# Kernel optimization log

Hardware: AMD Instinct MI355X
Metric: run time of the kernel (lower is better)

## Reference

```python
import jax, jax.numpy as jnp
import numpy as np

EPS = 1e-6

def setup_inputs() -> dict:
    key = jax.random.key(0)
    k1, k2, k3 = jax.random.split(key, 3)
    D = 1024
    return {
        "x": jax.random.normal(k1, (2, 2048, D), dtype=jnp.float32),
        "w_norm": jnp.ones((D,), dtype=jnp.float32),
        "w_qkv": jax.random.normal(k2, (3 * D, D), dtype=jnp.float32) * (1.0 / np.sqrt(D)),
        "w_out": jax.random.normal(k3, (D, D), dtype=jnp.float32) * (1.0 / np.sqrt(D)),
        "window_size": 128,
        "n_heads": 16,
    }

def reference(x, w_norm, w_qkv, w_out, window_size, n_heads):
    B, L, D = x.shape
    H = n_heads
    dh = D // H
    skip = x
    # RMSNorm
    rms = jnp.sqrt(jnp.mean(x * x, axis=-1, keepdims=True) + EPS)
    xn = w_norm * (x / rms)
    # QKV projection (torch Linear: y = x @ W.T)
    qkv = xn @ w_qkv.T  # [B, L, 3D]
    q, k, v = jnp.split(qkv, 3, axis=-1)
    q = q.reshape(B, L, H, dh).transpose(0, 2, 1, 3)  # [B,H,L,dh]
    k = k.reshape(B, L, H, dh).transpose(0, 2, 1, 3)
    v = v.reshape(B, L, H, dh).transpose(0, 2, 1, 3)
    scores = jnp.einsum("bhid,bhjd->bhij", q, k) / np.sqrt(dh)  # [B,H,L,L]
    # Symmetric window: token i attends to j in [i - w//2, i + w//2]
    idx = jnp.arange(L)
    half = window_size // 2
    band = jnp.abs(idx[:, None] - idx[None, :]) <= half  # [L, L]
    scores = jnp.where(band, scores, -jnp.inf)
    attn = jax.nn.softmax(scores, axis=-1)  # zeros outside band, matches torch loop
    out = jnp.einsum("bhij,bhjd->bhid", attn, v)  # [B,H,L,dh]
    out = out.transpose(0, 2, 1, 3).reshape(B, L, D)
    out = out @ w_out.T
    return out + skip
```

## Files before the change

kernel.cpp:

```cpp
#include <hip/hip_runtime.h>
#include <hip/hip_bf16.h>
#include <cstdint>

typedef float f32x4 __attribute__((ext_vector_type(4)));
typedef float f32x16 __attribute__((ext_vector_type(16)));
typedef short s16x8 __attribute__((ext_vector_type(8)));
typedef short s16x4 __attribute__((ext_vector_type(4)));
typedef unsigned int u32x2 __attribute__((ext_vector_type(2)));
typedef unsigned int u32x4 __attribute__((ext_vector_type(4)));

constexpr int B_ = 2, L_ = 2048, D_ = 1024, H_ = 16, DH = 64, HALF = 64;
constexpr int M_ROWS = B_ * L_;
constexpr int QKV_N = 3 * D_;

__device__ __forceinline__ void gload16(const void* g, void* l) {
    __builtin_amdgcn_global_load_lds(
        (const __attribute__((address_space(1))) unsigned int*)g,
        (__attribute__((address_space(3))) unsigned int*)l, 16, 0, 0);
}

__device__ __forceinline__ void cfence() {
    __builtin_amdgcn_sched_barrier(0);
    asm volatile("" ::: "memory");
}

__global__ __launch_bounds__(256) void prep_kernel(const float* __restrict__ x,
                                                   const float* __restrict__ wn,
                                                   const float* __restrict__ wq,
                                                   const float* __restrict__ wo,
                                                   __hip_bfloat16* __restrict__ xn,
                                                   __hip_bfloat16* __restrict__ oq,
                                                   __hip_bfloat16* __restrict__ oo) {
    constexpr int NQ4 = QKV_N * D_ / 4;
    constexpr int NCVT = NQ4 + D_ * D_ / 4;
    constexpr int CVTBLK = NCVT / 256;
    int bid = blockIdx.x;
    if (bid < CVTBLK) {
        int i = bid * 256 + threadIdx.x;
        const float* src; __hip_bfloat16* dst; int j;
        if (i < NQ4) { src = wq; dst = oq; j = i; }
        else         { src = wo; dst = oo; j = i - NQ4; }
        float4 v = reinterpret_cast<const float4*>(src)[j];
        s16x4 pk;
        float vals[4] = {v.x, v.y, v.z, v.w};
#pragma unroll
        for (int e = 0; e < 4; ++e) {
            __hip_bfloat16 t = __float2bfloat16(vals[e]);
            pk[e] = *reinterpret_cast<short*>(&t);
        }
        *(s16x4*)(dst + (size_t)j * 4) = pk;
    } else {
        int w = threadIdx.x >> 6, lane = threadIdx.x & 63;
        int row = (bid - CVTBLK) * 4 + w;
        const float4* xr = reinterpret_cast<const float4*>(x + (size_t)row * D_);
        const float4* wr = reinterpret_cast<const float4*>(wn);
        float4 v[4];
        float ss = 0.f;
#pragma unroll
        for (int c = 0; c < 4; ++c) {
            v[c] = xr[c * 64 + lane];
            ss += v[c].x * v[c].x + v[c].y * v[c].y + v[c].z * v[c].z + v[c].w * v[c].w;
        }
#pragma unroll
        for (int off = 32; off; off >>= 1) ss += __shfl_xor(ss, off);
        float rinv = rsqrtf(ss * (1.0f / D_) + 1e-6f);
#pragma unroll
        for (int c = 0; c < 4; ++c) {
            float4 wv = wr[c * 64 + lane];
            s16x4 pk;
            float vals[4] = {v[c].x * rinv * wv.x, v[c].y * rinv * wv.y,
                             v[c].z * rinv * wv.z, v[c].w * rinv * wv.w};
#pragma unroll
            for (int e = 0; e < 4; ++e) {
                __hip_bfloat16 t = __float2bfloat16(vals[e]);
                pk[e] = *reinterpret_cast<short*>(&t);
            }
            *(s16x4*)(xn + (size_t)row * D_ + (c * 64 + lane) * 4) = pk;
        }
    }
}

template <int EPI, int BN, int MINW>
__global__ __launch_bounds__(256, MINW) void gemm_pipe_kernel(const __hip_bfloat16* __restrict__ A,
                                                              const __hip_bfloat16* __restrict__ Bt,
                                                              __hip_bfloat16* __restrict__ Cbf,
                                                              __hip_bfloat16* __restrict__ vT,
                                                              float* __restrict__ Cf,
                                                              const float* __restrict__ resid,
                                                              int M, int N, int K) {
    constexpr int BM = 128;
    constexpr int NFR = BN / 32;
    constexpr int ATILE = BM * 64;
    constexpr int BTILE = BN * 64;
    constexpr int BUFB = ATILE + BTILE;
    constexpr int AISS = BM / 64, BISS = BN / 64;
    __shared__ __align__(16) char smem[4 * BUFB];

    const int tid = threadIdx.x;
    const int lane = tid & 63;
    const int wid = tid >> 6;

    int nwg = gridDim.x * gridDim.y;
    int lin = blockIdx.y * gridDim.x + blockIdx.x;
    int cpx = nwg >> 3;
    int swz = (lin & 7) * cpx + (lin >> 3);
    int bx = swz % gridDim.x;
    int by = swz / gridDim.x;

    const int rowBase = by * BM;
    const int colBase = bx * BN;
    const int NTILES = K >> 5;

    const int u = (tid & 7) ^ ((tid >> 3) & 7);
    const int sRow = 2 * (tid >> 3) + (u >> 2);
    const int sCol = (u & 3) * 8;
    const __hip_bfloat16* aG = A + (size_t)(rowBase + sRow) * K + sCol;
    const __hip_bfloat16* bG = Bt + (size_t)(colBase + sRow) * K + sCol;
    const int dstW = wid << 10;

    const int wm = wid >> 1, wn = wid & 1;
    const int l15 = lane & 15, hi = lane >> 4;
    const int sRd = (((l15 & 1) << 2) | hi) ^ ((l15 >> 1) & 7);
    const int aRd = wm * 4096 + (l15 >> 1) * 128 + sRd * 16;
    const int bRd = ATILE + wn * (BN * 32) + (l15 >> 1) * 128 + sRd * 16;

    f32x4 acc[4][NFR];
#pragma unroll
    for (int m = 0; m < 4; ++m)
#pragma unroll
        for (int n = 0; n < NFR; ++n) acc[m][n] = (f32x4){0.f, 0.f, 0.f, 0.f};

    auto STAGE = [&](int tt) {
        char* base = smem + ((tt & 3) * BUFB) + dstW;
        const __hip_bfloat16* as = aG + (size_t)tt * 32;
        const __hip_bfloat16* bs = bG + (size_t)tt * 32;
#pragma unroll
        for (int j = 0; j < AISS; ++j)
            gload16(as + (size_t)(j * 64) * K, base + j * 4096);
#pragma unroll
        for (int j = 0; j < BISS; ++j)
            gload16(bs + (size_t)(j * 64) * K, base + ATILE + j * 4096);
    };

    STAGE(0);
    STAGE(1);

    for (int t = 0; t < NTILES; ++t) {
        if (t + 2 < NTILES) {
            STAGE(t + 2);
            if constexpr (AISS + BISS == 4)
                asm volatile("s_waitcnt vmcnt(8)" ::: "memory");
            else
                asm volatile("s_waitcnt vmcnt(6)" ::: "memory");
        } else if (t + 1 < NTILES) {
            if constexpr (AISS + BISS == 4)
                asm volatile("s_waitcnt vmcnt(4)" ::: "memory");
            else
                asm volatile("s_waitcnt vmcnt(3)" ::: "memory");
        } else {
            asm volatile("s_waitcnt vmcnt(0)" ::: "memory");
        }
        asm volatile("s_waitcnt lgkmcnt(0)" ::: "memory");
        __builtin_amdgcn_s_barrier();
        cfence();

        const char* tb = smem + ((t & 3) * BUFB);
        s16x8 af[4], bf[NFR];
#pragma unroll
        for (int mf = 0; mf < 4; ++mf)
            af[mf] = *(const s16x8*)(tb + aRd + mf * 1024);
#pragma unroll
        for (int nf = 0; nf < NFR; ++nf)
            bf[nf] = *(const s16x8*)(tb + bRd + nf * 1024);

        __builtin_amdgcn_s_setprio(1);
#pragma unroll
        for (int mf = 0; mf < 4; ++mf)
#pragma unroll
            for (int nf = 0; nf < NFR; ++nf)
                acc[mf][nf] = __builtin_amdgcn_mfma_f32_16x16x32_bf16(af[mf], bf[nf],
                                                                      acc[mf][nf], 0, 0, 0);
        __builtin_amdgcn_s_setprio(0);
    }

    if constexpr (EPI == 0) {
        if (colBase < 2 * D_) {
#pragma unroll
            for (int mf = 0; mf < 4; ++mf)
#pragma unroll
                for (int nf = 0; nf < NFR; ++nf) {
                    int col = colBase + wn * (BN / 2) + nf * 16 + l15;
                    int row0 = rowBase + wm * 64 + mf * 16 + 4 * hi;
#pragma unroll
                    for (int r = 0; r < 4; ++r)
                        Cbf[(size_t)(row0 + r) * N + col] = __float2bfloat16(acc[mf][nf][r]);
                }
        } else {
            char* Ct = smem;
#pragma unroll
            for (int mf = 0; mf < 4; ++mf)
#pragma unroll
                for (int nf = 0; nf < NFR; ++nf) {
                    int cl = wn * (BN / 2) + nf * 16 + l15;
#pragma unroll
                    for (int r = 0; r < 4; ++r) {
                        int rl = wm * 64 + mf * 16 + 4 * hi + r;
                        __hip_bfloat16 t = __float2bfloat16(acc[mf][nf][r]);
                        *(short*)(Ct + cl * 272 + rl * 2) = *reinterpret_cast<short*>(&t);
                    }
                }
            __syncthreads();
            int cl = tid >> 1, half = tid & 1;
            int gcol = colBase + cl - 2 * D_;
            int hh = gcol >> 6, dd = gcol & 63;
            int bb2 = rowBase >> 11, i0 = rowBase & (L_ - 1);
            __hip_bfloat16* dstp = vT + ((size_t)(bb2 * H_ + hh) * DH + dd) * L_ + i0 + half * 64;
#pragma unroll
            for (int ch = 0; ch < 8; ++ch) {
                s16x8 vv = *(const s16x8*)(Ct + cl * 272 + half * 128 + ch * 16);
                *(s16x8*)(dstp + ch * 8) = vv;
            }
        }
    } else {
#pragma unroll
        for (int mf = 0; mf < 4; ++mf)
#pragma unroll
            for (int nf = 0; nf < NFR; ++nf) {
                int col = colBase + wn * (BN / 2) + nf * 16 + l15;
                int row0 = rowBase + wm * 64 + mf * 16 + 4 * hi;
#pragma unroll
                for (int r = 0; r < 4; ++r)
                    Cf[(size_t)(row0 + r) * N + col] = acc[mf][nf][r] + resid[(size_t)(row0 + r) * N + col];
            }
    }
}

__global__ __launch_bounds__(128, 2) void attn_mfma_kernel(const __hip_bfloat16* __restrict__ qkv,
                                                           const __hip_bfloat16* __restrict__ vT,
                                                           __hip_bfloat16* __restrict__ attn) {
    int tid = threadIdx.x;
    int w = tid >> 6;
    int lane = tid & 63;
    int l31 = lane & 31, hi1 = lane >> 5;
    int tq = blockIdx.x, h = blockIdx.y, b = blockIdx.z;
    int qbase = tq * 64 + 32 * w;
    int kb = qbase - HALF;
    int qg = qbase + l31;
    const __hip_bfloat16* qkvb = qkv + (size_t)(b * L_) * QKV_N;
    const __hip_bfloat16* vTg = vT + (size_t)(b * H_ + h) * DH * L_;

    s16x8 qf[4];
#pragma unroll
    for (int kk = 0; kk < 4; ++kk)
        qf[kk] = *(const s16x8*)(qkvb + (size_t)qg * QKV_N + h * DH + kk * 16 + hi1 * 8);

    f32x16 T[5];
#pragma unroll
    for (int kt = 0; kt < 5; ++kt) T[kt] = (f32x16)(0.f);
#pragma unroll
    for (int kt = 0; kt < 5; ++kt) {
        int keyg = kb + 32 * kt + l31;
        int kc = keyg < 0 ? 0 : (keyg > L_ - 1 ? L_ - 1 : keyg);
        const __hip_bfloat16* kp = qkvb + (size_t)kc * QKV_N + D_ + h * DH + hi1 * 8;
#pragma unroll
        for (int kk = 0; kk < 4; ++kk) {
            s16x8 kf = *(const s16x8*)(kp + kk * 16);
            T[kt] = __builtin_amdgcn_mfma_f32_32x32x16_bf16(kf, qf[kk], T[kt], 0, 0, 0);
        }
    }

    float mx = -1e30f;
#pragma unroll
    for (int kt = 0; kt < 5; ++kt) {
#pragma unroll
        for (int r = 0; r < 16; ++r) {
            int koff = (r & 3) + 8 * (r >> 2) + 4 * hi1;
            int keyg = kb + 32 * kt + koff;
            int del = keyg - qg;
            bool ok = (del >= -HALF) && (del <= HALF) && (keyg >= 0) && (keyg < L_);
            float t = ok ? T[kt][r] * 0.125f : -1e30f;
            T[kt][r] = t;
            mx = fmaxf(mx, t);
        }
    }
    mx = fmaxf(mx, __shfl_xor(mx, 32));
    float sum = 0.f;
#pragma unroll
    for (int kt = 0; kt < 5; ++kt) {
#pragma unroll
        for (int r = 0; r < 16; ++r) {
            float p = __expf(T[kt][r] - mx);
            T[kt][r] = p;
            sum += p;
        }
    }
    sum += __shfl_xor(sum, 32);
    float inv = 1.0f / sum;

    u32x4 pu[10];
#pragma unroll
    for (int kt = 0; kt < 5; ++kt) {
#pragma unroll
        for (int s = 0; s < 2; ++s) {
            unsigned P0, P1, P2, P3;
            asm("v_cvt_pk_bf16_f32 %0, %1, %2" : "=v"(P0) : "v"(T[kt][8 * s + 0]), "v"(T[kt][8 * s + 1]));
            asm("v_cvt_pk_bf16_f32 %0, %1, %2" : "=v"(P1) : "v"(T[kt][8 * s + 2]), "v"(T[kt][8 * s + 3]));
            asm("v_cvt_pk_bf16_f32 %0, %1, %2" : "=v"(P2) : "v"(T[kt][8 * s + 4]), "v"(T[kt][8 * s + 5]));
            asm("v_cvt_pk_bf16_f32 %0, %1, %2" : "=v"(P3) : "v"(T[kt][8 * s + 6]), "v"(T[kt][8 * s + 7]));
            u32x2 sA = __builtin_amdgcn_permlane32_swap(P0, P2, false, false);
            u32x2 sB = __builtin_amdgcn_permlane32_swap(P1, P3, false, false);
            pu[2 * kt + s] = (u32x4){sA[0], sB[0], sA[1], sB[1]};
        }
    }

    f32x16 O[2];
#pragma unroll
    for (int dt = 0; dt < 2; ++dt) O[dt] = (f32x16)(0.f);
#pragma unroll
    for (int t = 0; t < 10; ++t) {
        int kv = kb + 16 * t + 8 * hi1;
        kv = kv < 0 ? 0 : (kv > L_ - 8 ? L_ - 8 : kv);
        s16x8 pf = __builtin_bit_cast(s16x8, pu[t]);
#pragma unroll
        for (int dt = 0; dt < 2; ++dt) {
            s16x8 vf = *(const s16x8*)(vTg + (size_t)(32 * dt + l31) * L_ + kv);
            O[dt] = __builtin_amdgcn_mfma_f32_32x32x16_bf16(vf, pf, O[dt], 0, 0, 0);
        }
    }

    __hip_bfloat16* ob = attn + (size_t)(b * L_ + qg) * D_ + h * DH;
#pragma unroll
    for (int dt = 0; dt < 2; ++dt) {
#pragma unroll
        for (int rr = 0; rr < 4; ++rr) {
            s16x4 pk4;
#pragma unroll
            for (int j = 0; j < 4; ++j) {
                __hip_bfloat16 tb = __float2bfloat16(O[dt][4 * rr + j] * inv);
                pk4[j] = *reinterpret_cast<short*>(&tb);
            }
            *(s16x4*)(ob + 32 * dt + 8 * rr + 4 * hi1) = pk4;
        }
    }
}

extern "C" void kernel_launch(void* const* d_in, const int* in_sizes, int n_in,
                              void* d_out, int out_size, void* d_ws, size_t ws_size,
                              hipStream_t stream) {
    const float* x      = (const float*)d_in[0];
    const float* w_norm = (const float*)d_in[1];
    const float* w_qkv  = (const float*)d_in[2];
    const float* w_out  = (const float*)d_in[3];

    char* ws = (char*)d_ws;
    __hip_bfloat16* xn   = (__hip_bfloat16*)(ws);
    __hip_bfloat16* wq   = (__hip_bfloat16*)(ws + (8u  << 20));
    __hip_bfloat16* wo   = (__hip_bfloat16*)(ws + (14u << 20));
    __hip_bfloat16* qkv  = (__hip_bfloat16*)(ws + (16u << 20));
    __hip_bfloat16* attn = (__hip_bfloat16*)(ws + (40u << 20));
    __hip_bfloat16* vT   = (__hip_bfloat16*)(ws + (48u << 20));
    float* out = (float*)d_out;

    prep_kernel<<<4096 + M_ROWS / 4, 256, 0, stream>>>(x, w_norm, w_qkv, w_out, xn, wq, wo);

    gemm_pipe_kernel<0, 128, 2><<<dim3(QKV_N / 128, M_ROWS / 128), 256, 0, stream>>>(
        xn, wq, qkv, vT, nullptr, nullptr, M_ROWS, QKV_N, D_);

    attn_mfma_kernel<<<dim3(L_ / 64, H_, B_), 128, 0, stream>>>(qkv, vT, attn);

    gemm_pipe_kernel<1, 64, 3><<<dim3(D_ / 64, M_ROWS / 128), 256, 0, stream>>>(
        attn, wo, nullptr, nullptr, out, x, M_ROWS, D_, D_);
}
```

Before: 88.90 us.

## Enlarge QKV GEMM to 256x256 tiles with 512 threads and new LDS swizzle

Splits the templated GEMM into a dedicated QKV kernel and a projection kernel. The QKV kernel moves from 128x128 tiles with 256 threads to 256x256 tiles with 512 threads and 8x4 MFMA fragments per wave, which raises arithmetic intensity and cuts global and LDS traffic per flop. Its V-transpose epilogue now runs in two LDS passes. Both kernels switch to a new XOR swizzle for staging and fragment reads, aimed at LDS bank conflicts. The QKV grid shrinks to 12x16=192 blocks, and the 128 KB LDS footprint may limit occupancy, which risks leaving CUs underused on a large GPU.

```diff
diff --git a/kernel.cpp b/kernel.cpp
--- a/kernel.cpp
+++ b/kernel.cpp
@@ -80,20 +80,13 @@
     }
 }
 
-template <int EPI, int BN, int MINW>
-__global__ __launch_bounds__(256, MINW) void gemm_pipe_kernel(const __hip_bfloat16* __restrict__ A,
-                                                              const __hip_bfloat16* __restrict__ Bt,
-                                                              __hip_bfloat16* __restrict__ Cbf,
-                                                              __hip_bfloat16* __restrict__ vT,
-                                                              float* __restrict__ Cf,
-                                                              const float* __restrict__ resid,
-                                                              int M, int N, int K) {
-    constexpr int BM = 128;
-    constexpr int NFR = BN / 32;
-    constexpr int ATILE = BM * 64;
-    constexpr int BTILE = BN * 64;
-    constexpr int BUFB = ATILE + BTILE;
-    constexpr int AISS = BM / 64, BISS = BN / 64;
+__global__ __launch_bounds__(512, 2) void gemm_qkv_kernel(const __hip_bfloat16* __restrict__ A,
+                                                          const __hip_bfloat16* __restrict__ Bt,
+                                                          __hip_bfloat16* __restrict__ Cbf,
+                                                          __hip_bfloat16* __restrict__ vT,
+                                                          int M, int N, int K) {
+    constexpr int ATILE = 16384;
+    constexpr int BUFB = 32768;
     __shared__ __align__(16) char smem[4 * BUFB];
 
     const int tid = threadIdx.x;
@@ -107,56 +100,47 @@
     int bx = swz % gridDim.x;
     int by = swz / gridDim.x;
 
-    const int rowBase = by * BM;
-    const int colBase = bx * BN;
-    const int NTILES = K >> 5;
-
-    const int u = (tid & 7) ^ ((tid >> 3) & 7);
-    const int sRow = 2 * (tid >> 3) + (u >> 2);
-    const int sCol = (u & 3) * 8;
-    const __hip_bfloat16* aG = A + (size_t)(rowBase + sRow) * K + sCol;
-    const __hip_bfloat16* bG = Bt + (size_t)(colBase + sRow) * K + sCol;
+    const int rowBase = by * 256;
+    const int colBase = bx * 256;
+    const int NT = K >> 5;
+
+    const int r0 = tid >> 2;
+    const int cA = ((tid & 3) ^ ((r0 ^ (r0 >> 2)) & 3)) << 3;
+    const __hip_bfloat16* aG = A + (size_t)(rowBase + r0) * K + cA;
+    const __hip_bfloat16* bG = Bt + (size_t)(colBase + r0) * K + cA;
     const int dstW = wid << 10;
 
-    const int wm = wid >> 1, wn = wid & 1;
+    const int wm = wid >> 2, wn = wid & 3;
     const int l15 = lane & 15, hi = lane >> 4;
-    const int sRd = (((l15 & 1) << 2) | hi) ^ ((l15 >> 1) & 7);
-    const int aRd = wm * 4096 + (l15 >> 1) * 128 + sRd * 16;
-    const int bRd = ATILE + wn * (BN * 32) + (l15 >> 1) * 128 + sRd * 16;
-
-    f32x4 acc[4][NFR];
-#pragma unroll
-    for (int m = 0; m < 4; ++m)
-#pragma unroll
-        for (int n = 0; n < NFR; ++n) acc[m][n] = (f32x4){0.f, 0.f, 0.f, 0.f};
+    const int swzl = (l15 ^ (l15 >> 2)) & 3;
+    const int aRd = wm * 8192 + l15 * 64 + ((hi ^ swzl) << 4);
+    const int bRd = ATILE + wn * 4096 + l15 * 64 + ((hi ^ swzl) << 4);
+
+    f32x4 acc[8][4];
+#pragma unroll
+    for (int m = 0; m < 8; ++m)
+#pragma unroll
+        for (int n = 0; n < 4; ++n) acc[m][n] = (f32x4){0.f, 0.f, 0.f, 0.f};
 
     auto STAGE = [&](int tt) {
-        char* base = smem + ((tt & 3) * BUFB) + dstW;
+        char* base = smem + (tt & 3) * BUFB + dstW;
         const __hip_bfloat16* as = aG + (size_t)tt * 32;
         const __hip_bfloat16* bs = bG + (size_t)tt * 32;
-#pragma unroll
-        for (int j = 0; j < AISS; ++j)
-            gload16(as + (size_t)(j * 64) * K, base + j * 4096);
-#pragma unroll
-        for (int j = 0; j < BISS; ++j)
-            gload16(bs + (size_t)(j * 64) * K, base + ATILE + j * 4096);
+        gload16(as, base);
+        gload16(as + (size_t)128 * K, base + 8192);
+        gload16(bs, base + ATILE);
+        gload16(bs + (size_t)128 * K, base + ATILE + 8192);
     };
 
     STAGE(0);
     STAGE(1);
 
-    for (int t = 0; t < NTILES; ++t) {
-        if (t + 2 < NTILES) {
+    for (int t = 0; t < NT; ++t) {
+        if (t + 2 < NT) {
             STAGE(t + 2);
-            if constexpr (AISS + BISS == 4)
-                asm volatile("s_waitcnt vmcnt(8)" ::: "memory");
-            else
-                asm volatile("s_waitcnt vmcnt(6)" ::: "memory");
-        } else if (t + 1 < NTILES) {
-            if constexpr (AISS + BISS == 4)
-                asm volatile("s_waitcnt vmcnt(4)" ::: "memory");
-            else
-                asm volatile("s_waitcnt vmcnt(3)" ::: "memory");
+            asm volatile("s_waitcnt vmcnt(8)" ::: "memory");
+        } else if (t + 1 < NT) {
+            asm volatile("s_waitcnt vmcnt(4)" ::: "memory");
         } else {
             asm volatile("s_waitcnt vmcnt(0)" ::: "memory");
         }
@@ -164,75 +148,167 @@
         __builtin_amdgcn_s_barrier();
         cfence();
 
-        const char* tb = smem + ((t & 3) * BUFB);
-        s16x8 af[4], bf[NFR];
-#pragma unroll
-        for (int mf = 0; mf < 4; ++mf)
+        const char* tb = smem + (t & 3) * BUFB;
+        s16x8 af[8], bf[4];
+#pragma unroll
+        for (int mf = 0; mf < 8; ++mf)
             af[mf] = *(const s16x8*)(tb + aRd + mf * 1024);
 #pragma unroll
-        for (int nf = 0; nf < NFR; ++nf)
+        for (int nf = 0; nf < 4; ++nf)
             bf[nf] = *(const s16x8*)(tb + bRd + nf * 1024);
 
         __builtin_amdgcn_s_setprio(1);
 #pragma unroll
-        for (int mf = 0; mf < 4; ++mf)
-#pragma unroll
-            for (int nf = 0; nf < NFR; ++nf)
+        for (int mf = 0; mf < 8; ++mf)
+#pragma unroll
+            for (int nf = 0; nf < 4; ++nf)
                 acc[mf][nf] = __builtin_amdgcn_mfma_f32_16x16x32_bf16(af[mf], bf[nf],
                                                                       acc[mf][nf], 0, 0, 0);
         __builtin_amdgcn_s_setprio(0);
     }
 
-    if constexpr (EPI == 0) {
-        if (colBase < 2 * D_) {
-#pragma unroll
-            for (int mf = 0; mf < 4; ++mf)
-#pragma unroll
-                for (int nf = 0; nf < NFR; ++nf) {
-                    int col = colBase + wn * (BN / 2) + nf * 16 + l15;
-                    int row0 = rowBase + wm * 64 + mf * 16 + 4 * hi;
-#pragma unroll
-                    for (int r = 0; r < 4; ++r)
-                        Cbf[(size_t)(row0 + r) * N + col] = __float2bfloat16(acc[mf][nf][r]);
-                }
+    if (colBase < 2 * D_) {
+#pragma unroll
+        for (int mf = 0; mf < 8; ++mf)
+#pragma unroll
+            for (int nf = 0; nf < 4; ++nf) {
+                int col = colBase + wn * 64 + nf * 16 + l15;
+                int row0 = rowBase + wm * 128 + mf * 16 + 4 * hi;
+#pragma unroll
+                for (int r = 0; r < 4; ++r)
+                    Cbf[(size_t)(row0 + r) * N + col] = __float2bfloat16(acc[mf][nf][r]);
+            }
+    } else {
+        int bb2 = rowBase >> 11, i0 = rowBase & (L_ - 1);
+#pragma unroll
+        for (int p = 0; p < 2; ++p) {
+            if (p) __syncthreads();
+            if ((wn >> 1) == p) {
+#pragma unroll
+                for (int mf = 0; mf < 8; ++mf)
+#pragma unroll
+                    for (int nf = 0; nf < 4; ++nf) {
+                        int clp = (wn & 1) * 64 + nf * 16 + l15;
+#pragma unroll
+                        for (int r = 0; r < 4; ++r) {
+                            int rl = wm * 128 + mf * 16 + 4 * hi + r;
+                            __hip_bfloat16 t = __float2bfloat16(acc[mf][nf][r]);
+                            *(short*)(smem + clp * 528 + rl * 2) = *reinterpret_cast<short*>(&t);
+                        }
+                    }
+            }
+            __syncthreads();
+            {
+                int c = tid >> 2, qd = tid & 3;
+                int gcol = colBase + p * 128 + c - 2 * D_;
+                int hh = gcol >> 6, dd = gcol & 63;
+                __hip_bfloat16* dstp = vT + ((size_t)(bb2 * H_ + hh) * DH + dd) * L_ + i0 + qd * 64;
+#pragma unroll
+                for (int ch = 0; ch < 8; ++ch)
+                    *(s16x8*)(dstp + ch * 8) = *(const s16x8*)(smem + c * 528 + qd * 128 + ch * 16);
+            }
+        }
+    }
+}
+
+__global__ __launch_bounds__(256, 3) void gemm_proj_kernel(const __hip_bfloat16* __restrict__ A,
+                                                           const __hip_bfloat16* __restrict__ Bt,
+                                                           float* __restrict__ Cf,
+                                                           const float* __restrict__ resid,
+                                                           int M, int N, int K) {
+    constexpr int BM = 128, BN = 64;
+    constexpr int ATILE = BM * 64;
+    constexpr int BTILE = BN * 64;
+    constexpr int BUFB = ATILE + BTILE;
+    __shared__ __align__(16) char smem[4 * BUFB];
+
+    const int tid = threadIdx.x;
+    const int lane = tid & 63;
+    const int wid = tid >> 6;
+
+    int nwg = gridDim.x * gridDim.y;
+    int lin = blockIdx.y * gridDim.x + blockIdx.x;
+    int cpx = nwg >> 3;
+    int swz = (lin & 7) * cpx + (lin >> 3);
+    int bx = swz % gridDim.x;
+    int by = swz / gridDim.x;
+
+    const int rowBase = by * BM;
+    const int colBase = bx * BN;
+    const int NT = K >> 5;
+
+    const int r0 = tid >> 2;
+    const int cS = ((tid & 3) ^ ((r0 ^ (r0 >> 2)) & 3)) << 3;
+    const __hip_bfloat16* aG = A + (size_t)(rowBase + r0) * K + cS;
+    const __hip_bfloat16* bG = Bt + (size_t)(colBase + r0) * K + cS;
+    const int dstW = wid << 10;
+
+    const int wm = wid >> 1, wn = wid & 1;
+    const int l15 = lane & 15, hi = lane >> 4;
+    const int swzl = (l15 ^ (l15 >> 2)) & 3;
+    const int aRd = wm * 4096 + l15 * 64 + ((hi ^ swzl) << 4);
+    const int bRd = ATILE + wn * 2048 + l15 * 64 + ((hi ^ swzl) << 4);
+
+    f32x4 acc[4][2];
+#pragma unroll
+    for (int m = 0; m < 4; ++m)
+#pragma unroll
+        for (int n = 0; n < 2; ++n) acc[m][n] = (f32x4){0.f, 0.f, 0.f, 0.f};
+
+    auto STAGE = [&](int tt) {
+        char* base = smem + (tt & 3) * BUFB + dstW;
+        const __hip_bfloat16* as = aG + (size_t)tt * 32;
+        const __hip_bfloat16* bs = bG + (size_t)tt * 32;
+        gload16(as, base);
+        gload16(as + (size_t)64 * K, base + 4096);
+        gload16(bs, base + ATILE);
+    };
+
+    STAGE(0);
+    STAGE(1);
+
+    for (int t = 0; t < NT; ++t) {
+        if (t + 2 < NT) {
+            STAGE(t + 2);
+            asm volatile("s_waitcnt vmcnt(6)" ::: "memory");
+        } else if (t + 1 < NT) {
+            asm volatile("s_waitcnt vmcnt(3)" ::: "memory");
         } else {
-            char* Ct = smem;
-#pragma unroll
-            for (int mf = 0; mf < 4; ++mf)
-#pragma unroll
-                for (int nf = 0; nf < NFR; ++nf) {
-                    int cl = wn * (BN / 2) + nf * 16 + l15;
-#pragma unroll
-                    for (int r = 0; r < 4; ++r) {
-                        int rl = wm * 64 + mf * 16 + 4 * hi + r;
-                        __hip_bfloat16 t = __float2bfloat16(acc[mf][nf][r]);
-                        *(short*)(Ct + cl * 272 + rl * 2) = *reinterpret_cast<short*>(&t);
-                    }
-                }
-            __syncthreads();
-            int cl = tid >> 1, half = tid & 1;
-            int gcol = colBase + cl - 2 * D_;
-            int hh = gcol >> 6, dd = gcol & 63;
-            int bb2 = rowBase >> 11, i0 = rowBase & (L_ - 1);
-            __hip_bfloat16* dstp = vT + ((size_t)(bb2 * H_ + hh) * DH + dd) * L_ + i0 + half * 64;
-#pragma unroll
-            for (int ch = 0; ch < 8; ++ch) {
-                s16x8 vv = *(const s16x8*)(Ct + cl * 272 + half * 128 + ch * 16);
-                *(s16x8*)(dstp + ch * 8) = vv;
-            }
-        }
-    } else {
+            asm volatile("s_waitcnt vmcnt(0)" ::: "memory");
+        }
+        asm volatile("s_waitcnt lgkmcnt(0)" ::: "memory");
+        __builtin_amdgcn_s_barrier();
+        cfence();
+
+        const char* tb = smem + (t & 3) * BUFB;
+        s16x8 af[4], bf[2];
 #pragma unroll
         for (int mf = 0; mf < 4; ++mf)
-#pragma unroll
-            for (int nf = 0; nf < NFR; ++nf) {
-                int col = colBase + wn * (BN / 2) + nf * 16 + l15;
-                int row0 = rowBase + wm * 64 + mf * 16 + 4 * hi;
-#pragma unroll
-                for (int r = 0; r < 4; ++r)
-                    Cf[(size_t)(row0 + r) * N + col] = acc[mf][nf][r] + resid[(size_t)(row0 + r) * N + col];
-            }
-    }
+            af[mf] = *(const s16x8*)(tb + aRd + mf * 1024);
+#pragma unroll
+        for (int nf = 0; nf < 2; ++nf)
+            bf[nf] = *(const s16x8*)(tb + bRd + nf * 1024);
+
+        __builtin_amdgcn_s_setprio(1);
+#pragma unroll
+        for (int mf = 0; mf < 4; ++mf)
+#pragma unroll
+            for (int nf = 0; nf < 2; ++nf)
+                acc[mf][nf] = __builtin_amdgcn_mfma_f32_16x16x32_bf16(af[mf], bf[nf],
+                                                                      acc[mf][nf], 0, 0, 0);
+        __builtin_amdgcn_s_setprio(0);
+    }
+
+#pragma unroll
+    for (int mf = 0; mf < 4; ++mf)
+#pragma unroll
+        for (int nf = 0; nf < 2; ++nf) {
+            int col = colBase + wn * 32 + nf * 16 + l15;
+            int row0 = rowBase + wm * 64 + mf * 16 + 4 * hi;
+#pragma unroll
+            for (int r = 0; r < 4; ++r)
+                Cf[(size_t)(row0 + r) * N + col] = acc[mf][nf][r] + resid[(size_t)(row0 + r) * N + col];
+        }
 }
 
 __global__ __launch_bounds__(128, 2) void attn_mfma_kernel(const __hip_bfloat16* __restrict__ qkv,
@@ -363,11 +439,11 @@
 
     prep_kernel<<<4096 + M_ROWS / 4, 256, 0, stream>>>(x, w_norm, w_qkv, w_out, xn, wq, wo);
 
-    gemm_pipe_kernel<0, 128, 2><<<dim3(QKV_N / 128, M_ROWS / 128), 256, 0, stream>>>(
-        xn, wq, qkv, vT, nullptr, nullptr, M_ROWS, QKV_N, D_);
+    gemm_qkv_kernel<<<dim3(QKV_N / 256, M_ROWS / 256), 512, 0, stream>>>(
+        xn, wq, qkv, vT, M_ROWS, QKV_N, D_);
 
     attn_mfma_kernel<<<dim3(L_ / 64, H_, B_), 128, 0, stream>>>(qkv, vT, attn);
 
-    gemm_pipe_kernel<1, 64, 3><<<dim3(D_ / 64, M_ROWS / 128), 256, 0, stream>>>(
-        attn, wo, nullptr, nullptr, out, x, M_ROWS, D_, D_);
-}
+    gemm_proj_kernel<<<dim3(D_ / 64, M_ROWS / 128), 256, 0, stream>>>(
+        attn, wo, out, x, M_ROWS, D_, D_);
+}
```

Measured after the change: 89.91 us. About the same (+1.1%).
